# Performance work log

Measured on AMD Instinct MI355X. Metric: run time of the kernel, lower is better.

## Reference

```python
import jax, jax.numpy as jnp
import numpy as np

B, SQ, SK, D = 8, 4096, 4096, 64


def setup_inputs() -> dict:
    key = jax.random.key(0)
    k1, k2, k3 = jax.random.split(key, 3)
    x1 = jax.random.normal(k1, (B, SQ, D), dtype=jnp.float32)   # queries
    x2 = jax.random.normal(k2, (B, SK, D), dtype=jnp.float32)   # keys
    x3 = jax.random.normal(k3, (B, SK, D), dtype=jnp.float32)   # values
    x4 = 0                                                      # dropout p (static, 0 => deterministic)
    x5 = jnp.ones((1,), dtype=jnp.float32)                      # scale divisor
    return {"x1": x1, "x2": x2, "x3": x3, "x4": x4, "x5": x5}


def reference(x1, x2, x3, x4, x5):
    # scores: [B, Sq, Sk]
    scores = jnp.einsum("bqd,bkd->bqk", x1, x2) / x5
    attn = jax.nn.softmax(scores, axis=-1)
    p = float(x4)  # static python scalar
    if p > 0.0:
        mask = jax.random.bernoulli(jax.random.key(42), 1.0 - p, attn.shape)
        attn = attn * mask.astype(attn.dtype) / (1.0 - p)
    # out: [B, Sq, D]
    return jnp.einsum("bqk,bkd->bqd", attn, x3)
```

## Files before the change

kernel.cpp:

```cpp
#include <hip/hip_runtime.h>


typedef _Float16 f16x8 __attribute__((ext_vector_type(8)));
typedef _Float16 f16x4 __attribute__((ext_vector_type(4)));
typedef __fp16   h16x2 __attribute__((ext_vector_type(2)));
typedef float    f32x4 __attribute__((ext_vector_type(4)));
typedef float    f32x16 __attribute__((ext_vector_type(16)));

constexpr int kB  = 8;
constexpr int kSQ = 4096;
constexpr int kSK = 4096;
constexpr int kD  = 64;
constexpr int KSPLIT = 4;
constexpr int SKH = kSK / KSPLIT;
constexpr int BQ  = 256;
constexpr int MT  = 2;
constexpr int BK  = 64;
constexpr size_t APART = (size_t)kB * kSQ * kD;
constexpr float kLog2e = 1.44269504088896340736f;
constexpr float kDeferThr = 11.5f;

static __device__ __forceinline__ f16x4 pack4(float a, float b, float c, float d) {
    h16x2 p0 = __builtin_amdgcn_cvt_pkrtz(a, b);
    h16x2 p1 = __builtin_amdgcn_cvt_pkrtz(c, d);
    f16x4 r;
    r[0] = (_Float16)p0[0]; r[1] = (_Float16)p0[1];
    r[2] = (_Float16)p1[0]; r[3] = (_Float16)p1[1];
    return r;
}
static __device__ __forceinline__ f16x8 pack8(const float4& a, const float4& c) {
    f16x4 lo = pack4(a.x, a.y, a.z, a.w);
    f16x4 hi = pack4(c.x, c.y, c.z, c.w);
    f16x8 f;
    f[0] = lo[0]; f[1] = lo[1]; f[2] = lo[2]; f[3] = lo[3];
    f[4] = hi[0]; f[5] = hi[1]; f[6] = hi[2]; f[7] = hi[3];
    return f;
}
static __device__ __forceinline__ unsigned pkrtz_u(float a, float b) {
    union { h16x2 h; unsigned u; } cv;
    cv.h = __builtin_amdgcn_cvt_pkrtz(a, b);
    return cv.u;
}
static __device__ __forceinline__ float xhalf_max(float x) {
    union { float f; unsigned u; } uv; uv.f = x;
    auto pr = __builtin_amdgcn_permlane32_swap(uv.u, uv.u, false, false);
    union { unsigned u; float f; } r0, r1;
    r0.u = pr[0]; r1.u = pr[1];
    return fmaxf(r0.f, r1.f);
}

typedef const __attribute__((address_space(1))) unsigned int* gu32p;
typedef __attribute__((address_space(3))) unsigned int* lu32p;
static __device__ __forceinline__ void gload_lds16(const void* g, void* l) {
    __builtin_amdgcn_global_load_lds((gu32p)g, (lu32p)l, 16, 0, 0);
}

#define PA_SLICE(dst, sv, rb) do {                                          \
    unsigned c0 = pkrtz_u((sv)[(rb)+0], (sv)[(rb)+1]);                      \
    unsigned c1 = pkrtz_u((sv)[(rb)+2], (sv)[(rb)+3]);                      \
    unsigned c2 = pkrtz_u((sv)[(rb)+4], (sv)[(rb)+5]);                      \
    unsigned c3 = pkrtz_u((sv)[(rb)+6], (sv)[(rb)+7]);                      \
    auto r02 = __builtin_amdgcn_permlane32_swap(c0, c2, false, false);      \
    auto r13 = __builtin_amdgcn_permlane32_swap(c1, c3, false, false);      \
    union { unsigned u[4]; f16x8 v; } _r;                                   \
    _r.u[0] = r02[0]; _r.u[1] = r13[0]; _r.u[2] = r02[1]; _r.u[3] = r13[1]; \
    dst = _r.v;                                                             \
} while (0)

__global__ __launch_bounds__(256, 2)
void fattn_prepass(const float* __restrict__ Kg,
                   const float* __restrict__ Vg,
                   _Float16* __restrict__ Kh,
                   _Float16* __restrict__ Vt)
{
    __shared__ _Float16 tr[kD][BK];

    const int tid = threadIdx.x;
    const int kt  = blockIdx.x;
    const int b   = blockIdx.y;

    const int k = tid >> 2;
    const int p = tid & 3;
    const int gk = kt * BK + k;

    {
        const float* src = Kg + ((size_t)b * kSK + gk) * kD + p * 16;
        const float4 a0 = *(const float4*)(src + 0);
        const float4 a1 = *(const float4*)(src + 4);
        const float4 a2 = *(const float4*)(src + 8);
        const float4 a3 = *(const float4*)(src + 12);
        _Float16* dst = Kh + ((size_t)b * kSK + gk) * kD;
        const int fb0 = 2 * p, fb1 = 2 * p + 1;
        *(f16x8*)&dst[(fb0 ^ (gk & 7)) * 8] = pack8(a0, a1);
        *(f16x8*)&dst[(fb1 ^ (gk & 7)) * 8] = pack8(a2, a3);
    }
    {
        const float* src = Vg + ((size_t)b * kSK + gk) * kD + p * 16;
        const float4 a0 = *(const float4*)(src + 0);
        const float4 a1 = *(const float4*)(src + 4);
        const float4 a2 = *(const float4*)(src + 8);
        const float4 a3 = *(const float4*)(src + 12);
        const float v[16] = {a0.x,a0.y,a0.z,a0.w, a1.x,a1.y,a1.z,a1.w,
                             a2.x,a2.y,a2.z,a2.w, a3.x,a3.y,a3.z,a3.w};
#pragma unroll
        for (int j = 0; j < 16; ++j)
            tr[p * 16 + j][k] = (_Float16)v[j];
    }
    __syncthreads();
    {
        const int f  = tid >> 2;
        const int p2 = tid & 3;
        const f16x8 b0 = *(const f16x8*)&tr[f][p2 * 16 + 0];
        const f16x8 b1 = *(const f16x8*)&tr[f][p2 * 16 + 8];
        _Float16* dst = Vt + (((size_t)b * 64 + kt) * kD + f) * BK;
        const int kb0 = 2 * p2, kb1 = 2 * p2 + 1;
        *(f16x8*)&dst[(kb0 ^ (f & 7)) * 8] = b0;
        *(f16x8*)&dst[(kb1 ^ (f & 7)) * 8] = b1;
    }
}

__global__ __launch_bounds__(256, 2)
void fattn_partial(const float* __restrict__ Qg,
                   const _Float16* __restrict__ Kh,
                   const _Float16* __restrict__ Vt,
                   const float* __restrict__ sdiv,
                   _Float16* __restrict__ Ap,
                   float2* __restrict__ MLp)
{
    __shared__ __align__(16) _Float16 sK[2][BK * kD];
    __shared__ __align__(16) _Float16 sV[2][kD * BK];

    const int tid  = threadIdx.x;
    const int w    = tid >> 6;
    const int lane = tid & 63;
    const int l31  = lane & 31;
    const int hi   = lane >> 5;

    const int flat = blockIdx.x;
    const int c    = flat & 31;
    const int qi   = flat >> 5;
    const int b    = c >> 2;
    const int ks   = c & 3;
    const int qb   = qi * BQ;

    const float qscale = kLog2e / sdiv[0];

    const float* Qb = Qg + ((size_t)b * kSQ + qb) * kD;
    const _Float16* Khb = Kh + ((size_t)b * kSK + (size_t)ks * SKH) * kD;
    const _Float16* Vtb = Vt + (((size_t)b * 64 + (size_t)ks * (SKH / BK)) * kD) * BK;

    f16x8 qf[MT][4];
#pragma unroll
    for (int mt = 0; mt < MT; ++mt) {
        const float* qrow = Qb + (size_t)(w * 64 + mt * 32 + l31) * kD;
#pragma unroll
        for (int ds = 0; ds < 4; ++ds) {
            const float4 a  = *(const float4*)(qrow + ds * 16 + hi * 8);
            const float4 cc = *(const float4*)(qrow + ds * 16 + hi * 8 + 4);
            float4 as = make_float4(a.x * qscale, a.y * qscale, a.z * qscale, a.w * qscale);
            float4 cs = make_float4(cc.x * qscale, cc.y * qscale, cc.z * qscale, cc.w * qscale);
            qf[mt][ds] = pack8(as, cs);
        }
    }

    f16x8 ones;
#pragma unroll
    for (int j = 0; j < 8; ++j) ones[j] = (_Float16)1.0f;

    int offA[4];
#pragma unroll
    for (int i = 0; i < 4; ++i)
        offA[i] = l31 * 64 + (((2 * i + hi) ^ (l31 & 7)) * 8);

    auto stage = [&](int kt, int buf) {
        const char* gk = (const char*)(Khb + (size_t)kt * BK * kD) + w * 2048 + lane * 16;
        const char* gv = (const char*)(Vtb + (size_t)kt * kD * BK) + w * 2048 + lane * 16;
        char* lk = (char*)&sK[buf][0] + w * 2048;
        char* lv = (char*)&sV[buf][0] + w * 2048;
        gload_lds16(gk,        lk);
        gload_lds16(gk + 1024, lk + 1024);
        gload_lds16(gv,        lv);
        gload_lds16(gv + 1024, lv + 1024);
    };

    f32x16 oL[MT], oH[MT];
    f32x16 ol[MT];
    float m_i[MT];
#pragma unroll
    for (int mt = 0; mt < MT; ++mt) {
        m_i[mt] = -1e30f;
        ol[mt][0] = 0.0f;
#pragma unroll
        for (int r = 0; r < 16; ++r) { oL[mt][r] = 0.0f; oH[mt][r] = 0.0f; ol[mt][r] = 0.0f; }
    }

    stage(0, 0);
    __syncthreads();

    const int nIter = SKH / BK;
    for (int kt = 0; kt < nIter; ++kt) {
        const int buf = kt & 1;
        if (kt + 1 < nIter) stage(kt + 1, buf ^ 1);

        f16x8 kf0[4], kf1[4];
#pragma unroll
        for (int ds = 0; ds < 4; ++ds) {
            kf0[ds] = *(const f16x8*)&sK[buf][offA[ds]];
            kf1[ds] = *(const f16x8*)&sK[buf][offA[ds] + 2048];
        }

        f32x16 s0[MT], s1[MT];
#pragma unroll
        for (int mt = 0; mt < MT; ++mt)
#pragma unroll
            for (int r = 0; r < 16; ++r) { s0[mt][r] = 0.0f; s1[mt][r] = 0.0f; }

        __builtin_amdgcn_s_setprio(1);
#pragma unroll
        for (int ds = 0; ds < 4; ++ds)
#pragma unroll
            for (int mt = 0; mt < MT; ++mt) {
                s0[mt] = __builtin_amdgcn_mfma_f32_32x32x16_f16(kf0[ds], qf[mt][ds], s0[mt], 0, 0, 0);
                s1[mt] = __builtin_amdgcn_mfma_f32_32x32x16_f16(kf1[ds], qf[mt][ds], s1[mt], 0, 0, 0);
            }
        __builtin_amdgcn_s_setprio(0);

        f16x8 vf[4][2];
#pragma unroll
        for (int s = 0; s < 4; ++s) {
            vf[s][0] = *(const f16x8*)&sV[buf][offA[s]];
            vf[s][1] = *(const f16x8*)&sV[buf][offA[s] + 2048];
        }

#pragma unroll
        for (int mt = 0; mt < MT; ++mt) {
            float t[16];
#pragma unroll
            for (int r = 0; r < 16; ++r) t[r] = fmaxf(s0[mt][r], s1[mt][r]);
#pragma unroll
            for (int r = 0; r < 8; ++r)  t[r] = fmaxf(t[r], t[r + 8]);
#pragma unroll
            for (int r = 0; r < 4; ++r)  t[r] = fmaxf(t[r], t[r + 4]);
            float rm = fmaxf(fmaxf(t[0], t[1]), fmaxf(t[2], t[3]));
            rm = xhalf_max(rm);

            if (!__all(rm <= m_i[mt] + kDeferThr)) {
                const float mnew  = fmaxf(m_i[mt], rm);
                const float alpha = __builtin_amdgcn_exp2f(m_i[mt] - mnew);
                ol[mt][0] *= alpha;
#pragma unroll
                for (int r = 0; r < 16; ++r) { oL[mt][r] *= alpha; oH[mt][r] *= alpha; }
                m_i[mt] = mnew;
            }

#pragma unroll
            for (int r = 0; r < 16; ++r) {
                s0[mt][r] = __builtin_amdgcn_exp2f(s0[mt][r] - m_i[mt]);
                s1[mt][r] = __builtin_amdgcn_exp2f(s1[mt][r] - m_i[mt]);
            }

            f16x8 pa[4];
            PA_SLICE(pa[0], s0[mt], 0);
            PA_SLICE(pa[1], s0[mt], 8);
            PA_SLICE(pa[2], s1[mt], 0);
            PA_SLICE(pa[3], s1[mt], 8);

            __builtin_amdgcn_s_setprio(1);
#pragma unroll
            for (int s = 0; s < 4; ++s) {
                oL[mt] = __builtin_amdgcn_mfma_f32_32x32x16_f16(vf[s][0], pa[s], oL[mt], 0, 0, 0);
                oH[mt] = __builtin_amdgcn_mfma_f32_32x32x16_f16(vf[s][1], pa[s], oH[mt], 0, 0, 0);
                ol[mt] = __builtin_amdgcn_mfma_f32_32x32x16_f16(ones,     pa[s], ol[mt], 0, 0, 0);
            }
            __builtin_amdgcn_s_setprio(0);
        }

        __syncthreads();
    }

    _Float16* Ab = Ap + (size_t)ks * APART + ((size_t)b * kSQ + qb) * kD;
    float2* MLb = MLp + (size_t)ks * kB * kSQ + (size_t)b * kSQ + qb;
#pragma unroll
    for (int mt = 0; mt < MT; ++mt) {
        const int q = w * 64 + mt * 32 + l31;
        const float lf = ol[mt][0];
        const float inv = 1.0f / lf;
        _Float16* arow = &Ab[(size_t)q * kD];
#pragma unroll
        for (int g = 0; g < 4; ++g) {
            *(f16x4*)&arow[g * 8 + hi * 4] =
                pack4(oL[mt][4 * g] * inv, oL[mt][4 * g + 1] * inv,
                      oL[mt][4 * g + 2] * inv, oL[mt][4 * g + 3] * inv);
            *(f16x4*)&arow[32 + g * 8 + hi * 4] =
                pack4(oH[mt][4 * g] * inv, oH[mt][4 * g + 1] * inv,
                      oH[mt][4 * g + 2] * inv, oH[mt][4 * g + 3] * inv);
        }
        if (hi == 0) MLb[q] = make_float2(m_i[mt], lf);
    }
}

__global__ __launch_bounds__(256)
void fattn_combine(const _Float16* __restrict__ Ap,
                   const float2* __restrict__ MLp,
                   float* __restrict__ Og)
{
    const int idx = blockIdx.x * 256 + threadIdx.x;
    const int r = idx >> 4;
    const int c = (idx & 15) * 4;

    float m = -1e30f;
    float2 ml[KSPLIT];
#pragma unroll
    for (int s = 0; s < KSPLIT; ++s) {
        ml[s] = MLp[(size_t)s * kB * kSQ + r];
        m = fmaxf(m, ml[s].x);
    }
    float acc[4] = {0.f, 0.f, 0.f, 0.f};
    float lsum = 0.f;
#pragma unroll
    for (int s = 0; s < KSPLIT; ++s) {
        const float wgt = __builtin_amdgcn_exp2f(ml[s].x - m) * ml[s].y;
        lsum += wgt;
        const f16x4 a = *(const f16x4*)&Ap[(size_t)s * APART + (size_t)r * kD + c];
#pragma unroll
        for (int j = 0; j < 4; ++j) acc[j] += wgt * (float)a[j];
    }
    const float inv = 1.0f / lsum;
    float4 res = make_float4(acc[0] * inv, acc[1] * inv, acc[2] * inv, acc[3] * inv);
    *(float4*)&Og[(size_t)r * kD + c] = res;
}

extern "C" void kernel_launch(void* const* d_in, const int* in_sizes, int n_in,
                              void* d_out, int out_size, void* d_ws, size_t ws_size,
                              hipStream_t stream) {
    const float* Q    = (const float*)d_in[0];
    const float* K    = (const float*)d_in[1];
    const float* V    = (const float*)d_in[2];
    const float* sdiv = (const float*)d_in[4];
    float* O = (float*)d_out;

    _Float16* Kh  = (_Float16*)d_ws;
    _Float16* Vt  = Kh + (size_t)kB * kSK * kD;
    _Float16* Ap  = Vt + (size_t)kB * kSK * kD;
    float2*   MLp = (float2*)(Ap + (size_t)KSPLIT * APART);

    fattn_prepass<<<dim3(kSK / BK, kB), dim3(256), 0, stream>>>(K, V, Kh, Vt);
    fattn_partial<<<dim3((kSQ / BQ) * kB * KSPLIT), dim3(256), 0, stream>>>(Q, Kh, Vt, sdiv, Ap, MLp);
    fattn_combine<<<dim3(kB * kSQ * kD / (256 * 4)), dim3(256), 0, stream>>>(Ap, MLp, O);
}
```

Baseline: 133.8 us.

## Fuse split-K combine into partial kernel via last-arriver atomic ticket

Removes the separate combine kernel launch. Each partial block increments a per-(batch, query-tile) counter after a threadfence. The last of the KSPLIT blocks to arrive merges the partial outputs and writes the final fp32 result. Counters are zeroed in the prepass kernel. This saves a launch and its tail, at the cost of serialized combine work in the last-arriving blocks and extra fences and atomics.

```diff
diff --git a/kernel.cpp b/kernel.cpp
--- a/kernel.cpp
+++ b/kernel.cpp
@@ -16,6 +16,7 @@
 constexpr int BQ  = 256;
 constexpr int MT  = 2;
 constexpr int BK  = 64;
+constexpr int NQI = kSQ / BQ;
 constexpr size_t APART = (size_t)kB * kSQ * kD;
 constexpr float kLog2e = 1.44269504088896340736f;
 constexpr float kDeferThr = 11.5f;
@@ -71,13 +72,16 @@
 void fattn_prepass(const float* __restrict__ Kg,
                    const float* __restrict__ Vg,
                    _Float16* __restrict__ Kh,
-                   _Float16* __restrict__ Vt)
+                   _Float16* __restrict__ Vt,
+                   int* __restrict__ cnt)
 {
     __shared__ _Float16 tr[kD][BK];
 
     const int tid = threadIdx.x;
     const int kt  = blockIdx.x;
     const int b   = blockIdx.y;
+
+    if (kt == 0 && tid < NQI) cnt[b * NQI + tid] = 0;
 
     const int k = tid >> 2;
     const int p = tid & 3;
@@ -125,10 +129,13 @@
                    const _Float16* __restrict__ Vt,
                    const float* __restrict__ sdiv,
                    _Float16* __restrict__ Ap,
-                   float2* __restrict__ MLp)
+                   float2* __restrict__ MLp,
+                   int* __restrict__ cnt,
+                   float* __restrict__ Og)
 {
     __shared__ __align__(16) _Float16 sK[2][BK * kD];
     __shared__ __align__(16) _Float16 sV[2][kD * BK];
+    __shared__ int sTicket;
 
     const int tid  = threadIdx.x;
     const int w    = tid >> 6;
@@ -189,7 +196,6 @@
 #pragma unroll
     for (int mt = 0; mt < MT; ++mt) {
         m_i[mt] = -1e30f;
-        ol[mt][0] = 0.0f;
 #pragma unroll
         for (int r = 0; r < 16; ++r) { oL[mt][r] = 0.0f; oH[mt][r] = 0.0f; ol[mt][r] = 0.0f; }
     }
@@ -297,37 +303,39 @@
         }
         if (hi == 0) MLb[q] = make_float2(m_i[mt], lf);
     }
-}
-
-__global__ __launch_bounds__(256)
-void fattn_combine(const _Float16* __restrict__ Ap,
-                   const float2* __restrict__ MLp,
-                   float* __restrict__ Og)
-{
-    const int idx = blockIdx.x * 256 + threadIdx.x;
-    const int r = idx >> 4;
-    const int c = (idx & 15) * 4;
-
-    float m = -1e30f;
-    float2 ml[KSPLIT];
-#pragma unroll
-    for (int s = 0; s < KSPLIT; ++s) {
-        ml[s] = MLp[(size_t)s * kB * kSQ + r];
-        m = fmaxf(m, ml[s].x);
-    }
-    float acc[4] = {0.f, 0.f, 0.f, 0.f};
-    float lsum = 0.f;
-#pragma unroll
-    for (int s = 0; s < KSPLIT; ++s) {
-        const float wgt = __builtin_amdgcn_exp2f(ml[s].x - m) * ml[s].y;
-        lsum += wgt;
-        const f16x4 a = *(const f16x4*)&Ap[(size_t)s * APART + (size_t)r * kD + c];
-#pragma unroll
-        for (int j = 0; j < 4; ++j) acc[j] += wgt * (float)a[j];
-    }
-    const float inv = 1.0f / lsum;
-    float4 res = make_float4(acc[0] * inv, acc[1] * inv, acc[2] * inv, acc[3] * inv);
-    *(float4*)&Og[(size_t)r * kD + c] = res;
+
+    __threadfence();
+    if (tid == 0) sTicket = atomicAdd(&cnt[b * NQI + qi], 1);
+    __syncthreads();
+    if (sTicket == KSPLIT - 1) {
+        __threadfence();
+        const size_t rowb = (size_t)b * kSQ + qb;
+        const int cc = (tid & 15) * 4;
+#pragma unroll 1
+        for (int p = 0; p < 16; ++p) {
+            const int rr = (tid >> 4) + p * 16;
+            float2 ml[KSPLIT];
+            float m = -1e30f;
+#pragma unroll
+            for (int s = 0; s < KSPLIT; ++s) {
+                ml[s] = MLp[(size_t)s * kB * kSQ + rowb + rr];
+                m = fmaxf(m, ml[s].x);
+            }
+            float acc[4] = {0.f, 0.f, 0.f, 0.f};
+            float lsum = 0.f;
+#pragma unroll
+            for (int s = 0; s < KSPLIT; ++s) {
+                const float wgt = __builtin_amdgcn_exp2f(ml[s].x - m) * ml[s].y;
+                lsum += wgt;
+                const f16x4 a = *(const f16x4*)&Ap[(size_t)s * APART + (rowb + rr) * kD + cc];
+#pragma unroll
+                for (int j = 0; j < 4; ++j) acc[j] += wgt * (float)a[j];
+            }
+            const float inv = 1.0f / lsum;
+            float4 res = make_float4(acc[0] * inv, acc[1] * inv, acc[2] * inv, acc[3] * inv);
+            *(float4*)&Og[(rowb + rr) * kD + cc] = res;
+        }
+    }
 }
 
 extern "C" void kernel_launch(void* const* d_in, const int* in_sizes, int n_in,
@@ -343,8 +351,8 @@
     _Float16* Vt  = Kh + (size_t)kB * kSK * kD;
     _Float16* Ap  = Vt + (size_t)kB * kSK * kD;
     float2*   MLp = (float2*)(Ap + (size_t)KSPLIT * APART);
-
-    fattn_prepass<<<dim3(kSK / BK, kB), dim3(256), 0, stream>>>(K, V, Kh, Vt);
-    fattn_partial<<<dim3((kSQ / BQ) * kB * KSPLIT), dim3(256), 0, stream>>>(Q, Kh, Vt, sdiv, Ap, MLp);
-    fattn_combine<<<dim3(kB * kSQ * kD / (256 * 4)), dim3(256), 0, stream>>>(Ap, MLp, O);
-}
+    int*      cnt = (int*)(MLp + (size_t)KSPLIT * kB * kSQ);
+
+    fattn_prepass<<<dim3(kSK / BK, kB), dim3(256), 0, stream>>>(K, V, Kh, Vt, cnt);
+    fattn_partial<<<dim3((kSQ / BQ) * kB * KSPLIT), dim3(256), 0, stream>>>(Q, Kh, Vt, sdiv, Ap, MLp, cnt, O);
+}
```

Measured after the change: 227.8 us. 1.7x slower.
